# Kernel tuning notes

Hardware: AMD Instinct MI355X
Metric: run time of the kernel (lower is better)

Reference implementation:

```python
import jax, jax.numpy as jnp
import numpy as np

THRESHOLD = 0.5     # overlap_thresh
NEG_POS = 3         # negative:positive ratio
VAR = (0.1, 0.2)    # cfg['variance']


def point_form(pr):
    # cxcywh -> xmin,ymin,xmax,ymax
    return jnp.concatenate([pr[:, :2] - pr[:, 2:] / 2, pr[:, :2] + pr[:, 2:] / 2], axis=1)


def jaccard(a, b):
    # a: [N,4] point-form truths, b: [P,4] point-form priors -> IoU [N,P]
    lt = jnp.maximum(a[:, None, :2], b[None, :, :2])
    rb = jnp.minimum(a[:, None, 2:], b[None, :, 2:])
    wh = jnp.clip(rb - lt, 0.0)
    inter = wh[..., 0] * wh[..., 1]
    area_a = ((a[:, 2] - a[:, 0]) * (a[:, 3] - a[:, 1]))[:, None]
    area_b = ((b[:, 2] - b[:, 0]) * (b[:, 3] - b[:, 1]))[None, :]
    return inter / (area_a + area_b - inter)


def encode(matched, priors):
    # matched: [P,4] point-form, priors: [P,4] cxcywh
    g_cxcy = ((matched[:, :2] + matched[:, 2:]) / 2 - priors[:, :2]) / (VAR[0] * priors[:, 2:])
    g_wh = jnp.log((matched[:, 2:] - matched[:, :2]) / priors[:, 2:]) / VAR[1]
    return jnp.concatenate([g_cxcy, g_wh], axis=1)


def match_one(truths, labels, priors):
    # truths [N,4], labels [N], priors [P,4] cxcywh
    N = truths.shape[0]
    P = priors.shape[0]
    overlaps = jaccard(truths, point_form(priors))          # [N,P]
    best_prior_idx = jnp.argmax(overlaps, axis=1)           # [N] best prior per truth
    best_truth_overlap = jnp.max(overlaps, axis=0)          # [P]
    best_truth_idx = jnp.argmax(overlaps, axis=0)           # [P]
    # ensure each truth's best prior is kept (overlap forced to 2)
    best_truth_overlap = best_truth_overlap.at[best_prior_idx].set(2.0)
    hit = best_prior_idx[:, None] == jnp.arange(P)[None, :]  # [N,P]
    chosen = jnp.max(jnp.where(hit, jnp.arange(N)[:, None], -1), axis=0)
    best_truth_idx = jnp.where(chosen >= 0, chosen, best_truth_idx)
    matched = truths[best_truth_idx]                        # [P,4]
    conf = labels[best_truth_idx].astype(jnp.int32) + 1
    conf = jnp.where(best_truth_overlap < THRESHOLD, 0, conf)
    return encode(matched, priors), conf


def smooth_l1(x):
    ax = jnp.abs(x)
    return jnp.where(ax < 1.0, 0.5 * ax * ax, ax - 0.5)


def multibox_loss(loc_data, conf_data, priors, targets):
    num, P, C = conf_data.shape
    truths = targets[..., :4]
    labels = targets[..., 4]
    loc_t, conf_t = jax.vmap(match_one, in_axes=(0, 0, None))(truths, labels, priors)
    pos = conf_t > 0                                        # [B,P]

    # localization loss over positives
    loss_l = jnp.sum(jnp.where(pos[..., None], smooth_l1(loc_data - loc_t), 0.0))

    # hard-negative mining score: logsumexp - conf[label clamped to {0,1}]
    batch_conf = jax.lax.stop_gradient(conf_data).reshape(-1, C)
    conf_flat = conf_t.reshape(-1)
    clamped = jnp.where(conf_flat != 0, 1, conf_flat)
    # replicate torch nonzero()-indexing quirk: row 0 also set to 1 if any positive exists
    clamped = clamped.at[0].set(jnp.where(jnp.any(conf_flat != 0), 1, clamped[0]))
    lse = jax.scipy.special.logsumexp(batch_conf, axis=1)
    loss_c = lse - jnp.take_along_axis(batch_conf, clamped[:, None], axis=1)[:, 0]
    loss_c = loss_c.reshape(num, P)
    loss_c = jnp.where(pos, 0.0, loss_c)
    # rank of each prior by descending mining loss
    idx_rank = jnp.argsort(jnp.argsort(-loss_c, axis=1), axis=1)
    num_pos = jnp.sum(pos.astype(jnp.int32), axis=1, keepdims=True)  # [B,1]
    num_neg = jnp.clip(NEG_POS * num_pos, None, P - 1)
    neg = idx_rank < num_neg
    sel = pos | neg

    # confidence cross-entropy over selected priors, original labels as targets
    logp = jax.nn.log_softmax(conf_data, axis=-1)           # [B,P,C]
    ce = -jnp.take_along_axis(logp, conf_t[..., None], axis=-1)[..., 0]
    loss_conf = jnp.sum(jnp.where(sel, ce, 0.0))

    Nf = jnp.sum(num_pos).astype(jnp.float32)
    return loss_l / Nf, loss_conf / Nf


def setup_inputs() -> dict:
    key = jax.random.key(0)
    k1, k2, k3, k4, k5, k6, k7 = jax.random.split(key, 7)
    B, P, C, NOBJ = 128, 8732, 21, 20
    loc_data = jax.random.normal(k1, (B, P, 4), jnp.float32)
    conf_data = jax.random.normal(k2, (B, P, C), jnp.float32)
    pcxy = jax.random.uniform(k3, (P, 2), jnp.float32, 0.05, 0.95)
    pwh = jax.random.uniform(k4, (P, 2), jnp.float32, 0.05, 0.4)
    priors = jnp.concatenate([pcxy, pwh], axis=1)           # cxcywh
    mins = jax.random.uniform(k5, (B, NOBJ, 2), jnp.float32, 0.0, 0.6)
    wh = jax.random.uniform(k6, (B, NOBJ, 2), jnp.float32, 0.05, 0.35)
    lab = jax.random.randint(k7, (B, NOBJ), 0, C - 1).astype(jnp.float32)
    targets = jnp.concatenate([mins, mins + wh, lab[..., None]], axis=-1)
    return {"loc_data": loc_data, "conf_data": conf_data, "priors": priors, "targets": targets}


def reference(loc_data, conf_data, priors, targets):
    return multibox_loss(loc_data, conf_data, priors, targets)
```

## Files before the change

kernel.cpp:

```cpp
#include <hip/hip_runtime.h>

#define PP 8732
#define NB 20
#define NC 21
#define BTH 256
#define CHP 512
#define NCH 18
#define NLS 9
#define BTS 1024
#define NWS (BTS/64)

__device__ __forceinline__ float sl1(float d){
  float a = fabsf(d);
  return a < 1.0f ? 0.5f*a*a : a - 0.5f;
}

__device__ __forceinline__ float wave_max64(float x){
  int t;
  t = __builtin_amdgcn_update_dpp(0, __float_as_int(x), 0x111, 0xF, 0xF, true); x = fmaxf(x, __int_as_float(t));
  t = __builtin_amdgcn_update_dpp(0, __float_as_int(x), 0x112, 0xF, 0xF, true); x = fmaxf(x, __int_as_float(t));
  t = __builtin_amdgcn_update_dpp(0, __float_as_int(x), 0x114, 0xF, 0xF, true); x = fmaxf(x, __int_as_float(t));
  t = __builtin_amdgcn_update_dpp(0, __float_as_int(x), 0x118, 0xF, 0xF, true); x = fmaxf(x, __int_as_float(t));
  t = __builtin_amdgcn_update_dpp(0, __float_as_int(x), 0x142, 0xF, 0xF, true); x = fmaxf(x, __int_as_float(t));
  t = __builtin_amdgcn_update_dpp(0, __float_as_int(x), 0x143, 0xF, 0xF, true); x = fmaxf(x, __int_as_float(t));
  return __int_as_float(__builtin_amdgcn_readlane(__float_as_int(x), 63));
}

__device__ __forceinline__ int wave_sum64_lane63(int x){
  x += __builtin_amdgcn_update_dpp(0, x, 0x111, 0xF, 0xF, true);
  x += __builtin_amdgcn_update_dpp(0, x, 0x112, 0xF, 0xF, true);
  x += __builtin_amdgcn_update_dpp(0, x, 0x114, 0xF, 0xF, true);
  x += __builtin_amdgcn_update_dpp(0, x, 0x118, 0xF, 0xF, true);
  x += __builtin_amdgcn_update_dpp(0, x, 0x142, 0xF, 0xF, true);
  x += __builtin_amdgcn_update_dpp(0, x, 0x143, 0xF, 0xF, true);
  return x;
}

extern "C" __global__ void __launch_bounds__(BTH, 8)
mb_main(const float* __restrict__ conf_data,
        const float* __restrict__ priors,
        const float* __restrict__ targets,
        float* __restrict__ rankneg,
        unsigned char* __restrict__ meta,
        unsigned long long* __restrict__ keys2)
{
  const int b = blockIdx.x, y = blockIdx.y;
  const int tid = threadIdx.x, lane = tid & 63, wid = tid >> 6;

  __shared__ __align__(16) float s_buf[4][64*NC];
  __shared__ unsigned long long s_keys[4][NB];

  if (y >= NCH){
    const int wbase = (y - NCH)*1024 + wid*256;
    char* l0 = (char*)&s_buf[wid][0];
    for (int g=0; g<4; ++g){
      const int q0 = wbase + g*64;
      const int cnt = (q0 < PP) ? ((PP - q0 < 64) ? (PP - q0) : 64) : 0;
      if (cnt == 64){
        asm volatile("s_waitcnt lgkmcnt(0)" ::: "memory");
        const char* gp = (const char*)(conf_data + ((long)b*PP + q0)*NC) + lane*16;
        #pragma unroll
        for (int i=0;i<5;i++)
          __builtin_amdgcn_global_load_lds(
            (const __attribute__((address_space(1))) void*)(gp + i*1024),
            (__attribute__((address_space(3))) void*)(l0 + i*1024), 16, 0, 0);
        if (lane < 16)
          __builtin_amdgcn_global_load_lds(
            (const __attribute__((address_space(1))) void*)(gp + 5*1024),
            (__attribute__((address_space(3))) void*)(l0 + 5*1024), 16, 0, 0);
        asm volatile("s_waitcnt vmcnt(0)" ::: "memory");

        const float* v = s_buf[wid] + lane*NC;
        float vv[NC];
        #pragma unroll
        for (int c=0;c<NC;c++) vv[c] = v[c];
        float m = vv[0];
        #pragma unroll
        for (int c=1;c<NC;c++) m = fmaxf(m, vv[c]);
        float s = 0.f;
        #pragma unroll
        for (int c=0;c<NC;c++) s += __expf(vv[c]-m);
        rankneg[(long)b*PP + q0 + lane] = __logf(s) + m - vv[0];
      } else if (cnt > 0){
        asm volatile("s_waitcnt lgkmcnt(0)" ::: "memory");
        const float4* cb4 = reinterpret_cast<const float4*>(conf_data + ((long)b*PP + q0)*NC);
        float4* sb4 = reinterpret_cast<float4*>(s_buf[wid]);
        const int tot4 = (cnt*NC) >> 2;
        for (int i=lane; i<tot4; i+=64) sb4[i] = cb4[i];
        asm volatile("s_waitcnt vmcnt(0) lgkmcnt(0)" ::: "memory");
        if (lane < cnt){
          const float* v = s_buf[wid] + lane*NC;
          float vv[NC];
          #pragma unroll
          for (int c=0;c<NC;c++) vv[c] = v[c];
          float m = vv[0];
          #pragma unroll
          for (int c=1;c<NC;c++) m = fmaxf(m, vv[c]);
          float s = 0.f;
          #pragma unroll
          for (int c=0;c<NC;c++) s += __expf(vv[c]-m);
          rankneg[(long)b*PP + q0 + lane] = __logf(s) + m - vv[0];
        }
      }
    }
    return;
  }

  const int chunk = y;
  const int q0w = chunk*CHP + wid*128;
  const int p0  = q0w + 2*lane;

  const float* tb = targets + (long)b*NB*5;

  unsigned long long mykey = 0ULL;

  if (q0w < PP){
    float bx1[2], by1[2], bx2[2], by2[2], areab[2];
    #pragma unroll
    for (int i=0;i<2;i++){
      int p = p0 + i;
      int pc = (p < PP) ? p : 0;
      float4 pr = reinterpret_cast<const float4*>(priors)[pc];
      float x1 = pr.x - pr.z*0.5f, y1 = pr.y - pr.w*0.5f;
      float x2 = pr.x + pr.z*0.5f, y2 = pr.y + pr.w*0.5f;
      if (p >= PP){ x1=3e9f; y1=3e9f; x2=3e9f; y2=3e9f; }
      bx1[i]=x1; by1[i]=y1; bx2[i]=x2; by2[i]=y2;
      areab[i] = (x2-x1)*(y2-y1);
    }

    float bestov[2] = {-1.f,-1.f};
    int   bestn [2] = {0,0};

    #pragma unroll
    for (int n=0;n<NB;n++){
      const float t_x = tb[n*5+0];
      const float t_y = tb[n*5+1];
      const float t_z = tb[n*5+2];
      const float t_w = tb[n*5+3];
      const float aa  = (t_z-t_x)*(t_w-t_y);
      float candiou = -1.0f; unsigned candp = 0u;
      #pragma unroll
      for (int i=0;i<2;i++){
        float lx=fmaxf(t_x,bx1[i]), ly=fmaxf(t_y,by1[i]);
        float rx=fminf(t_z,bx2[i]), ry=fminf(t_w,by2[i]);
        float iw=fmaxf(rx-lx,0.f), ih=fmaxf(ry-ly,0.f);
        float inter = iw*ih;
        float iou = inter * __builtin_amdgcn_rcpf(aa + areab[i] - inter);
        if (iou > bestov[i]){ bestov[i]=iou; bestn[i]=n; }
        if (iou > candiou){ candiou=iou; candp=(unsigned)(p0+i); }
      }
      float wmax = wave_max64(candiou);
      unsigned long long mk = __ballot(candiou == wmax);
      int wlane = __ffsll((long long)mk) - 1;
      unsigned wp = (unsigned)__builtin_amdgcn_readlane((int)candp, wlane);
      unsigned long long key = ((unsigned long long)__float_as_uint(wmax)<<32)
                             | (unsigned long long)(0xFFFFFFFFu - wp);
      if (lane == n) mykey = key;
    }

    if (p0 < PP){
      unsigned short mb =
          (unsigned short)( ((bestn[0]<<1) | (bestov[0] >= 0.5f ? 1 : 0))
                          | (((bestn[1]<<1) | (bestov[1] >= 0.5f ? 1 : 0)) << 8) );
      *reinterpret_cast<unsigned short*>(meta + (long)b*PP + p0) = mb;
    }
  }

  if (lane < NB) s_keys[wid][lane] = mykey;
  __syncthreads();
  if (tid < NB){
    unsigned long long mx = s_keys[0][tid];
    #pragma unroll
    for (int w=1;w<4;w++) if (s_keys[w][tid] > mx) mx = s_keys[w][tid];
    keys2[((long)b*NCH + chunk)*NB + tid] = mx;
  }
}

extern "C" __global__ void __launch_bounds__(BTS)
mb_select(const float* __restrict__ loc_data,
          const float* __restrict__ conf_data,
          const float* __restrict__ priors,
          const float* __restrict__ targets,
          const float* __restrict__ rankneg,
          const unsigned char* __restrict__ meta,
          const unsigned long long* __restrict__ keys2,
          float* __restrict__ rowres, int* __restrict__ ticket,
          float* __restrict__ out, int Bn)
{
  const int b = blockIdx.x, tid = threadIdx.x, lane = tid & 63, wid = tid >> 6;
  __shared__ __align__(16) float s_val[PP];
  __shared__ __align__(16) unsigned int s_meta4[PP/4];
  __shared__ float4 s_tr4[NB];
  __shared__ float s_lab[NB];
  __shared__ int   s_bp[NB];
  __shared__ int   s_tot[32];
  __shared__ float s_fa[NWS], s_fb[NWS], s_fc[NWS];
  __shared__ int   s_ia[NWS];
  __shared__ float s_rowll, s_rowpc;
  __shared__ int   s_npos, s_last;
  unsigned char* s_meta = (unsigned char*)s_meta4;
  float4* sv4 = reinterpret_cast<float4*>(s_val);

  const float4* rr = reinterpret_cast<const float4*>(rankneg + (long)b*PP);
  for (int i=tid;i<PP/4;i+=BTS) sv4[i]=rr[i];
  const unsigned int* mr = reinterpret_cast<const unsigned int*>(meta + (long)b*PP);
  for (int i=tid;i<PP/4;i+=BTS) s_meta4[i]=mr[i];
  if (tid < NB*5){
    int n = tid/5, k2 = tid-n*5;
    float vv = targets[((long)b*NB+n)*5+k2];
    if (k2<4) ((float*)&s_tr4[n])[k2]=vv; else s_lab[n]=vv;
  }
  if (tid < NB){
    unsigned long long mx = 0ULL;
    #pragma unroll
    for (int c=0;c<NCH;c++){
      unsigned long long kk = keys2[((long)b*NCH + c)*NB + tid];
      if (kk > mx) mx = kk;
    }
    s_bp[tid] = (int)(0xFFFFFFFFu - (unsigned)(mx & 0xFFFFFFFFULL));
  }
  if (tid < 32) s_tot[tid] = 0;
  __syncthreads();

  if (tid==0){
    for (int n=0;n<NB;n++) s_meta[s_bp[n]] = (unsigned char)((n<<1)|1);
  }
  __syncthreads();

  float4 rv0 = sv4[tid];
  float4 rv1 = sv4[tid+1024];
  float4 rv2 = (tid < PP/4-2048) ? sv4[tid+2048] : make_float4(0.f,0.f,0.f,0.f);
  unsigned mm0 = s_meta4[tid];
  unsigned mm1 = s_meta4[tid+1024];
  unsigned mm2 = (tid < PP/4-2048) ? s_meta4[tid+2048] : 0u;
  if (mm0 & 0x00000001u) rv0.x = 0.f;
  if (mm0 & 0x00000100u) rv0.y = 0.f;
  if (mm0 & 0x00010000u) rv0.z = 0.f;
  if (mm0 & 0x01000000u) rv0.w = 0.f;
  if (mm1 & 0x00000001u) rv1.x = 0.f;
  if (mm1 & 0x00000100u) rv1.y = 0.f;
  if (mm1 & 0x00010000u) rv1.z = 0.f;
  if (mm1 & 0x01000000u) rv1.w = 0.f;
  if (mm2 & 0x00000001u) rv2.x = 0.f;
  if (mm2 & 0x00000100u) rv2.y = 0.f;
  if (mm2 & 0x00010000u) rv2.z = 0.f;
  if (mm2 & 0x01000000u) rv2.w = 0.f;

  int spec = 0; float delta = 0.f, val0 = 0.f;
  if (b==0 && tid==0 && !(mm0 & 1u)){
    float v0 = conf_data[0], v1 = conf_data[1];
    float r0 = rv0.x;
    float r0p = r0 + v0 - v1;
    delta = r0 - r0p;
    spec = 1;
    rv0.x = r0p; val0 = r0p;
  }

  float ll=0.f, pc=0.f; int np=0;
  for (int p=tid;p<PP;p+=BTS){
    int mt = s_meta[p];
    if (mt & 1){
      np++;
      int n = mt>>1;
      int ct = (int)s_lab[n] + 1;
      const float* cp = conf_data + ((long)b*PP+p)*NC;
      float v0 = cp[0], vct = cp[ct];
      pc += s_val[p] + v0 - vct;
      float4 t = s_tr4[n];
      float4 prr = reinterpret_cast<const float4*>(priors)[p];
      float4 ld = reinterpret_cast<const float4*>(loc_data)[(long)b*PP+p];
      float g0 = ((t.x+t.z)*0.5f - prr.x)/(0.1f*prr.z);
      float g1 = ((t.y+t.w)*0.5f - prr.y)/(0.1f*prr.w);
      float g2 = __logf((t.z-t.x)/prr.z)/0.2f;
      float g3 = __logf((t.w-t.y)/prr.w)/0.2f;
      ll += sl1(ld.x-g0)+sl1(ld.y-g1)+sl1(ld.z-g2)+sl1(ld.w-g3);
    }
  }
  #pragma unroll
  for (int o=32;o;o>>=1){
    ll += __shfl_down(ll,o,64);
    pc += __shfl_down(pc,o,64);
    np += __shfl_down(np,o,64);
  }
  if (lane==0){ s_fa[wid]=ll; s_fb[wid]=pc; s_ia[wid]=np; }
  __syncthreads();
  if (tid==0){
    float a=0.f,c2=0.f; int ni=0;
    for (int w=0;w<NWS;w++){ a+=s_fa[w]; c2+=s_fb[w]; ni+=s_ia[w]; }
    s_rowll=a; s_rowpc=c2; s_npos=ni;
  }
  __syncthreads();
  const int num_pos = s_npos;
  int k = num_pos*3; if (k > PP-1) k = PP-1;

  float negsum = 0.f;
  if (k > 0){
    unsigned lo=0u, hi=0x7f800000u;
    int it=0;
    while (lo < hi){
      unsigned mid = lo + ((hi - lo + 1u) >> 1);
      int c = (__float_as_uint(rv0.x)>=mid) + (__float_as_uint(rv0.y)>=mid)
            + (__float_as_uint(rv0.z)>=mid) + (__float_as_uint(rv0.w)>=mid)
            + (__float_as_uint(rv1.x)>=mid) + (__float_as_uint(rv1.y)>=mid)
            + (__float_as_uint(rv1.z)>=mid) + (__float_as_uint(rv1.w)>=mid)
            + (__float_as_uint(rv2.x)>=mid) + (__float_as_uint(rv2.y)>=mid)
            + (__float_as_uint(rv2.z)>=mid) + (__float_as_uint(rv2.w)>=mid);
      c = wave_sum64_lane63(c);
      if (lane==63) atomicAdd(&s_tot[it], c);
      __syncthreads();
      int tot = s_tot[it];
      if (tot >= k) lo = mid; else hi = mid - 1u;
      it++;
    }
    const unsigned vstar = lo;

    int cg=0; float sg=0.f;
    #define ACC(x) if (__float_as_uint(x)>vstar){cg++;sg+=(x);}
    ACC(rv0.x) ACC(rv0.y) ACC(rv0.z) ACC(rv0.w)
    ACC(rv1.x) ACC(rv1.y) ACC(rv1.z) ACC(rv1.w)
    ACC(rv2.x) ACC(rv2.y) ACC(rv2.z) ACC(rv2.w)
    #undef ACC
    #pragma unroll
    for (int o=32;o;o>>=1){ cg += __shfl_down(cg,o,64); sg += __shfl_down(sg,o,64); }
    __syncthreads();
    if (lane==0){ s_ia[wid]=cg; s_fa[wid]=sg; }
    __syncthreads();
    if (tid==0){
      int cG=0; float sumG=0.f;
      for (int w=0;w<NWS;w++){ cG+=s_ia[w]; sumG+=s_fa[w]; }
      int tie = k - cG;
      negsum = sumG + (float)tie * __uint_as_float(vstar);
      if (b==0 && spec && __float_as_uint(val0) >= vstar) negsum += delta;
    }
  }

  if (tid==0){
    rowres[b*4+0] = s_rowll;
    rowres[b*4+1] = s_rowpc + negsum;
    rowres[b*4+2] = (float)num_pos;
    __threadfence();
    int t = atomicAdd(ticket, 1);
    s_last = (t == Bn - 1) ? 1 : 0;
  }
  __syncthreads();

  if (s_last){
    __threadfence();
    float a0=0.f, a1=0.f, a2=0.f;
    for (int i=tid;i<Bn;i+=BTS){
      a0 += rowres[i*4+0]; a1 += rowres[i*4+1]; a2 += rowres[i*4+2];
    }
    #pragma unroll
    for (int o=32;o;o>>=1){
      a0 += __shfl_down(a0,o,64);
      a1 += __shfl_down(a1,o,64);
      a2 += __shfl_down(a2,o,64);
    }
    if (lane==0){ s_fa[wid]=a0; s_fb[wid]=a1; s_fc[wid]=a2; }
    __syncthreads();
    if (tid==0){
      float A0=0.f,A1=0.f,A2=0.f;
      for (int w=0;w<NWS;w++){ A0+=s_fa[w]; A1+=s_fb[w]; A2+=s_fc[w]; }
      out[0] = A0/A2;
      out[1] = A1/A2;
    }
  }
}

extern "C" void kernel_launch(void* const* d_in, const int* in_sizes, int n_in,
                              void* d_out, int out_size, void* d_ws, size_t ws_size,
                              hipStream_t stream) {
  const float* loc     = (const float*)d_in[0];
  const float* conf    = (const float*)d_in[1];
  const float* priors  = (const float*)d_in[2];
  const float* targets = (const float*)d_in[3];
  float* out = (float*)d_out;
  int B = in_sizes[0] / (PP*4);

  char* ws = (char*)d_ws;
  int*   ticket = (int*)ws;
  float* rowres = (float*)(ws + 64);
  unsigned long long* keys2 = (unsigned long long*)(ws + 4096);
  size_t off_rank = (4096 + (size_t)B*NCH*NB*8 + 255) & ~(size_t)255;
  float* rankneg = (float*)(ws + off_rank);
  unsigned char* metaa = (unsigned char*)(ws + off_rank + (size_t)B*PP*4);

  hipMemsetAsync(d_ws, 0, 64, stream);
  hipLaunchKernelGGL(mb_main,   dim3(B, NCH+NLS), dim3(BTH), 0, stream,
                     conf, priors, targets, rankneg, metaa, keys2);
  hipLaunchKernelGGL(mb_select, dim3(B), dim3(BTS), 0, stream,
                     loc, conf, priors, targets, rankneg, metaa, keys2,
                     rowres, ticket, out, B);
}
```

Measured before the change: 206.9 us.

## Double-buffer LDS staging of conf rows in the log-sum-exp branch

In the blocks that compute per-prior log-sum-exp, each wave now holds two LDS buffers. It issues the asynchronous global-to-LDS loads for the next 64-prior group while it computes the current group, using partial vmcnt waits so load latency overlaps compute. Full 256-prior groups take this pipelined path, and the tail keeps the old serial path. The LDS allocation doubles for every block of the kernel, which can lower how many blocks fit on a CU, including the matching blocks.

New measurement: 210.3 us. About the same (+1.6%).

```diff
diff --git a/kernel.cpp b/kernel.cpp
--- a/kernel.cpp
+++ b/kernel.cpp
@@ -34,6 +34,32 @@
   x += __builtin_amdgcn_update_dpp(0, x, 0x142, 0xF, 0xF, true);
   x += __builtin_amdgcn_update_dpp(0, x, 0x143, 0xF, 0xF, true);
   return x;
+}
+
+__device__ __forceinline__ void stage64(const float* gbase, char* lds, int lane){
+  const char* gp = (const char*)gbase + lane*16;
+  #pragma unroll
+  for (int i=0;i<5;i++)
+    __builtin_amdgcn_global_load_lds(
+      (const __attribute__((address_space(1))) void*)(gp + i*1024),
+      (__attribute__((address_space(3))) void*)(lds + i*1024), 16, 0, 0);
+  if (lane < 16)
+    __builtin_amdgcn_global_load_lds(
+      (const __attribute__((address_space(1))) void*)(gp + 5*1024),
+      (__attribute__((address_space(3))) void*)(lds + 5*1024), 16, 0, 0);
+}
+
+__device__ __forceinline__ float lse_from_lds(const float* v){
+  float vv[NC];
+  #pragma unroll
+  for (int c=0;c<NC;c++) vv[c] = v[c];
+  float m = vv[0];
+  #pragma unroll
+  for (int c=1;c<NC;c++) m = fmaxf(m, vv[c]);
+  float s = 0.f;
+  #pragma unroll
+  for (int c=0;c<NC;c++) s += __expf(vv[c]-m);
+  return __logf(s) + m - vv[0];
 }
 
 extern "C" __global__ void __launch_bounds__(BTH, 8)
@@ -47,59 +73,46 @@
   const int b = blockIdx.x, y = blockIdx.y;
   const int tid = threadIdx.x, lane = tid & 63, wid = tid >> 6;
 
-  __shared__ __align__(16) float s_buf[4][64*NC];
+  __shared__ __align__(16) float s_buf[4][2][64*NC];
   __shared__ unsigned long long s_keys[4][NB];
 
   if (y >= NCH){
     const int wbase = (y - NCH)*1024 + wid*256;
-    char* l0 = (char*)&s_buf[wid][0];
-    for (int g=0; g<4; ++g){
-      const int q0 = wbase + g*64;
-      const int cnt = (q0 < PP) ? ((PP - q0 < 64) ? (PP - q0) : 64) : 0;
-      if (cnt == 64){
-        asm volatile("s_waitcnt lgkmcnt(0)" ::: "memory");
-        const char* gp = (const char*)(conf_data + ((long)b*PP + q0)*NC) + lane*16;
-        #pragma unroll
-        for (int i=0;i<5;i++)
-          __builtin_amdgcn_global_load_lds(
-            (const __attribute__((address_space(1))) void*)(gp + i*1024),
-            (__attribute__((address_space(3))) void*)(l0 + i*1024), 16, 0, 0);
-        if (lane < 16)
-          __builtin_amdgcn_global_load_lds(
-            (const __attribute__((address_space(1))) void*)(gp + 5*1024),
-            (__attribute__((address_space(3))) void*)(l0 + 5*1024), 16, 0, 0);
-        asm volatile("s_waitcnt vmcnt(0)" ::: "memory");
-
-        const float* v = s_buf[wid] + lane*NC;
-        float vv[NC];
-        #pragma unroll
-        for (int c=0;c<NC;c++) vv[c] = v[c];
-        float m = vv[0];
-        #pragma unroll
-        for (int c=1;c<NC;c++) m = fmaxf(m, vv[c]);
-        float s = 0.f;
-        #pragma unroll
-        for (int c=0;c<NC;c++) s += __expf(vv[c]-m);
-        rankneg[(long)b*PP + q0 + lane] = __logf(s) + m - vv[0];
-      } else if (cnt > 0){
-        asm volatile("s_waitcnt lgkmcnt(0)" ::: "memory");
-        const float4* cb4 = reinterpret_cast<const float4*>(conf_data + ((long)b*PP + q0)*NC);
-        float4* sb4 = reinterpret_cast<float4*>(s_buf[wid]);
-        const int tot4 = (cnt*NC) >> 2;
-        for (int i=lane; i<tot4; i+=64) sb4[i] = cb4[i];
-        asm volatile("s_waitcnt vmcnt(0) lgkmcnt(0)" ::: "memory");
-        if (lane < cnt){
-          const float* v = s_buf[wid] + lane*NC;
-          float vv[NC];
-          #pragma unroll
-          for (int c=0;c<NC;c++) vv[c] = v[c];
-          float m = vv[0];
-          #pragma unroll
-          for (int c=1;c<NC;c++) m = fmaxf(m, vv[c]);
-          float s = 0.f;
-          #pragma unroll
-          for (int c=0;c<NC;c++) s += __expf(vv[c]-m);
-          rankneg[(long)b*PP + q0 + lane] = __logf(s) + m - vv[0];
+    char* lb[2] = { (char*)&s_buf[wid][0][0], (char*)&s_buf[wid][1][0] };
+    const float* gb = conf_data + (long)b*PP*NC;
+
+    if (wbase + 256 <= PP){
+      stage64(gb + (long)(wbase)*NC, lb[0], lane);
+      #pragma unroll
+      for (int g=0; g<4; ++g){
+        if (g < 3){
+          asm volatile("s_waitcnt lgkmcnt(0)" ::: "memory");
+          stage64(gb + (long)(wbase + (g+1)*64)*NC, lb[(g+1)&1], lane);
+        }
+        if (g == 0)      asm volatile("s_waitcnt vmcnt(6)" ::: "memory");
+        else if (g < 3)  asm volatile("s_waitcnt vmcnt(7)" ::: "memory");
+        else             asm volatile("s_waitcnt vmcnt(1)" ::: "memory");
+        rankneg[(long)b*PP + wbase + g*64 + lane] =
+            lse_from_lds(s_buf[wid][g&1] + lane*NC);
+      }
+    } else {
+      for (int g=0; g<4; ++g){
+        const int q0 = wbase + g*64;
+        const int cnt = (q0 < PP) ? ((PP - q0 < 64) ? (PP - q0) : 64) : 0;
+        if (cnt == 64){
+          asm volatile("s_waitcnt lgkmcnt(0)" ::: "memory");
+          stage64(gb + (long)q0*NC, lb[0], lane);
+          asm volatile("s_waitcnt vmcnt(0)" ::: "memory");
+          rankneg[(long)b*PP + q0 + lane] = lse_from_lds(s_buf[wid][0] + lane*NC);
+        } else if (cnt > 0){
+          asm volatile("s_waitcnt lgkmcnt(0)" ::: "memory");
+          const float4* cb4 = reinterpret_cast<const float4*>(gb + (long)q0*NC);
+          float4* sb4 = reinterpret_cast<float4*>(s_buf[wid][0]);
+          const int tot4 = (cnt*NC) >> 2;
+          for (int i=lane; i<tot4; i+=64) sb4[i] = cb4[i];
+          asm volatile("s_waitcnt vmcnt(0) lgkmcnt(0)" ::: "memory");
+          if (lane < cnt)
+            rankneg[(long)b*PP + q0 + lane] = lse_from_lds(s_buf[wid][0] + lane*NC);
         }
       }
     }
```
